# Performance work log

Measured on AMD Instinct MI355X. Metric: run time of the kernel, lower is better.

Reference implementation:

```python
import jax, jax.numpy as jnp
import numpy as np

B, D, K = 8, 128, 7          # batch, num objects, per-object feature
Q = 256                      # question embedding size
G0, G1 = 511, 512            # g-layer sizes
F1, F2, OUT = 512, 1024, 16  # f-layer sizes


def setup_inputs() -> dict:
    key = jax.random.key(0)
    ks = jax.random.split(key, 14)
    def lin(kw, kb, fan_in, fan_out):
        lim = 1.0 / np.sqrt(fan_in)
        w = jax.random.uniform(kw, (fan_in, fan_out), jnp.float32, -lim, lim)
        b = jax.random.uniform(kb, (fan_out,), jnp.float32, -lim, lim)
        return w, b
    x = jax.random.normal(ks[0], (B, D, K), jnp.float32)
    qst = jax.random.normal(ks[1], (B, Q), jnp.float32)
    g0_w, g0_b = lin(ks[2], ks[3], 2 * K, G0)
    g1_w, g1_b = lin(ks[4], ks[5], G0 + Q, G1)
    f1_w, f1_b = lin(ks[6], ks[7], G1, F1)
    f2_w, f2_b = lin(ks[8], ks[9], F1, F2)
    f3_w, f3_b = lin(ks[10], ks[11], F2, OUT)
    return {"x": x, "qst": qst,
            "g0_w": g0_w, "g0_b": g0_b, "g1_w": g1_w, "g1_b": g1_b,
            "f1_w": f1_w, "f1_b": f1_b, "f2_w": f2_w, "f2_b": f2_b,
            "f3_w": f3_w, "f3_b": f3_b}


def reference(x, qst, g0_w, g0_b, g1_w, g1_b, f1_w, f1_b, f2_w, f2_b, f3_w, f3_b):
    b, d, k = x.shape
    # all-pairs: torch x_i[b,a,c,:]=x[b,c,:], x_j[b,a,c,:]=x[b,a,:]
    x_i = jnp.broadcast_to(x[:, None, :, :], (b, d, d, k))
    x_j = jnp.broadcast_to(x[:, :, None, :], (b, d, d, k))
    pairs = jnp.concatenate([x_i, x_j], axis=-1)            # (b,d,d,2k)
    h = jax.nn.relu(pairs @ g0_w + g0_b)                    # (b,d,d,G0)
    q = jnp.broadcast_to(qst[:, None, None, :], (b, d, d, qst.shape[-1]))
    h = jnp.concatenate([h, q], axis=-1)                    # (b,d,d,G0+Q)
    h = jax.nn.relu(h @ g1_w + g1_b)                        # (b,d,d,G1)
    x_g = h.sum(axis=(1, 2))                                # sum over d^2 pairs -> (b,G1)
    f = jax.nn.relu(x_g @ f1_w + f1_b)
    f = jax.nn.relu(f @ f2_w + f2_b)                        # dropout = identity (eval)
    logits = f @ f3_w + f3_b
    return jax.nn.log_softmax(logits, axis=1)
```

## Files before the change

kernel.cpp:

```cpp
#include <hip/hip_runtime.h>
#include <hip/hip_bf16.h>

#define B_  8
#define D_  128
#define K_  7
#define Q_  256
#define G0_ 511
#define G0P 512
#define G1_ 512
#define F1_ 512
#define F2_ 1024
#define OUT_ 16

typedef __bf16 bf16x8 __attribute__((ext_vector_type(8)));
typedef float  f32x4  __attribute__((ext_vector_type(4)));

#define GL2LDS(g, l) __builtin_amdgcn_global_load_lds(                        \
    (const __attribute__((address_space(1))) void*)(g),                       \
    (__attribute__((address_space(3))) void*)(l), 16, 0, 0)

__global__ void k_prep(const float* __restrict__ x, const float* __restrict__ g0w,
                       const float* __restrict__ g0b, const float* __restrict__ qst,
                       const float* __restrict__ g1w, const float* __restrict__ g1b,
                       float* __restrict__ u, float* __restrict__ v,
                       __bf16* __restrict__ w1t, float* __restrict__ qterm,
                       float* __restrict__ xg) {
    const int blk = blockIdx.x;
    const int t   = threadIdx.x;
    if (blk < 1024) {
        __shared__ float xs[8];
        if (t < K_) xs[t] = x[blk * K_ + t];
        __syncthreads();
        #pragma unroll
        for (int h = 0; h < 2; ++h) {
            const int g = t + h * 256;
            float su = 0.f, sv = 0.f;
            if (g < G0_) {
                #pragma unroll
                for (int k = 0; k < K_; ++k) {
                    su += xs[k] * g0w[k * G0_ + g];
                    sv += xs[k] * g0w[(K_ + k) * G0_ + g];
                }
                su += g0b[g];
            }
            u[blk * G0P + g] = (g < G0_) ? su : 0.f;
            v[blk * G0P + g] = (g < G0_) ? sv : 0.f;
        }
    } else if (blk < 1280) {
        __shared__ __bf16 tile[32][33];
        const int bb = blk - 1024;
        const int bx = bb & 15, by = bb >> 4;
        const int r = t >> 5, c = t & 31;
        #pragma unroll
        for (int i = 0; i < 4; ++i) {
            const int k = by * 32 + r + i * 8;
            const int n = bx * 32 + c;
            tile[r + i * 8][c] = (__bf16)((k < G0_) ? g1w[k * G1_ + n] : 0.f);
        }
        __syncthreads();
        #pragma unroll
        for (int i = 0; i < 4; ++i) {
            const int n = bx * 32 + r + i * 8;
            const int cc = (c >> 3) & 3, j = c & 7;
            const int slot = cc ^ ((n >> 1) & 3);
            w1t[by * 16384 + n * 32 + slot * 8 + j] = tile[c][r + i * 8];
        }
    } else if (blk < 1312) {
        __shared__ float qs[256];
        __shared__ float red[2][128];
        const int qb = blk - 1280;
        const int b = qb >> 2, nb = (qb & 3) << 7;
        qs[t] = qst[b * Q_ + t];
        __syncthreads();
        const int n = nb + (t & 127);
        const int qh = (t >> 7) * 128;
        float s = 0.f;
        #pragma unroll 8
        for (int q = 0; q < 128; ++q)
            s += qs[qh + q] * g1w[(G0_ + qh + q) * G1_ + n];
        red[t >> 7][t & 127] = s;
        __syncthreads();
        if (t < 128)
            qterm[b * G1_ + nb + t] = red[0][t] + red[1][t] + g1b[nb + t];
    } else {
        const int b = blk - 1312;
        xg[b * G1_ + t] = 0.f;
        xg[b * G1_ + 256 + t] = 0.f;
    }
}

__global__ __launch_bounds__(256, 2)
void k_pair(const float* __restrict__ u, const float* __restrict__ v,
            const __bf16* __restrict__ w1t, const float* __restrict__ qterm,
            float* __restrict__ xg) {
    __shared__ float  v_a[512];
    __shared__ __bf16 At[2][4096];
    __shared__ __bf16 Bt[2][8192];
    __shared__ float  ebuf[4][128];

    const int bid  = blockIdx.x;
    const int b    = bid >> 8;
    const int a    = (bid >> 1) & 127;
    const int nbase = (bid & 1) << 8;
    const int tid  = threadIdx.x;
    const int wave = tid >> 6, lane = tid & 63;
    const int quad = lane >> 4, l15 = lane & 15;
    const int nloc = (wave >> 1) * 128;
    const int mtg  = (wave & 1) * 4;
    const int swz  = (l15 >> 1) & 3;

    if (tid < 128)
        *(float4*)(v_a + tid * 4) = *(const float4*)(v + (b * D_ + a) * G0P + tid * 4);

    const int iw0 = wave * 4;
    const __bf16* gsrc = w1t + (size_t)(nbase + iw0 * 16 + (lane >> 2)) * 32
                             + (lane & 3) * 8;

    const int sm = tid >> 1;
    const int sk = (tid & 1) << 4;
    const float* urow = u + (b * D_ + sm) * G0P + sk;
    const int woff = (sm >> 4) * 512 + (sk >> 3) * 128 + (sm & 15) * 8;

    f32x4 acc[4][8];
    #pragma unroll
    for (int mt = 0; mt < 4; ++mt)
        #pragma unroll
        for (int nt = 0; nt < 8; ++nt)
            acc[mt][nt] = (f32x4){0.f, 0.f, 0.f, 0.f};

    float4 u0, u1, u2, u3;
    auto load_u = [&](int kq) {
        const float* p = urow + kq * 32;
        u0 = *(const float4*)p;       u1 = *(const float4*)(p + 4);
        u2 = *(const float4*)(p + 8); u3 = *(const float4*)(p + 12);
    };
    auto stage_B = [&](int buf, int kq) {
        const __bf16* g = gsrc + kq * 16384;
        __bf16* l = &Bt[buf][iw0 * 512];
        #pragma unroll
        for (int j = 0; j < 4; ++j)
            GL2LDS(g + j * 512, l + j * 512);
    };
    auto write_A = [&](int buf, int kq) {
        const float* vp = v_a + kq * 32 + sk;
        const float4 v0 = *(const float4*)vp,       v1 = *(const float4*)(vp + 4);
        const float4 v2 = *(const float4*)(vp + 8), v3 = *(const float4*)(vp + 12);
        bf16x8 h0, h1;
        h0[0] = (__bf16)fmaxf(u0.x + v0.x, 0.f);
        h0[1] = (__bf16)fmaxf(u0.y + v0.y, 0.f);
        h0[2] = (__bf16)fmaxf(u0.z + v0.z, 0.f);
        h0[3] = (__bf16)fmaxf(u0.w + v0.w, 0.f);
        h0[4] = (__bf16)fmaxf(u1.x + v1.x, 0.f);
        h0[5] = (__bf16)fmaxf(u1.y + v1.y, 0.f);
        h0[6] = (__bf16)fmaxf(u1.z + v1.z, 0.f);
        h0[7] = (__bf16)fmaxf(u1.w + v1.w, 0.f);
        h1[0] = (__bf16)fmaxf(u2.x + v2.x, 0.f);
        h1[1] = (__bf16)fmaxf(u2.y + v2.y, 0.f);
        h1[2] = (__bf16)fmaxf(u2.z + v2.z, 0.f);
        h1[3] = (__bf16)fmaxf(u2.w + v2.w, 0.f);
        h1[4] = (__bf16)fmaxf(u3.x + v3.x, 0.f);
        h1[5] = (__bf16)fmaxf(u3.y + v3.y, 0.f);
        h1[6] = (__bf16)fmaxf(u3.z + v3.z, 0.f);
        h1[7] = (__bf16)fmaxf(u3.w + v3.w, 0.f);
        __bf16* w = &At[buf][woff];
        *(bf16x8*)w = h0;
        *(bf16x8*)(w + 128) = h1;
    };

    stage_B(0, 0);
    load_u(0);
    __syncthreads();
    write_A(0, 0);
    __syncthreads();

    for (int kq = 0; kq < 16; ++kq) {
        const int buf = kq & 1;
        if (kq < 15) {
            stage_B(buf ^ 1, kq + 1);
            load_u(kq + 1);
        }
        bf16x8 af[4];
        #pragma unroll
        for (int mt = 0; mt < 4; ++mt)
            af[mt] = *(const bf16x8*)&At[buf][(mtg + mt) * 512 + lane * 8];
        bf16x8 bfr[8];
        const __bf16* btb = &Bt[buf][(nloc + l15) * 32 + ((quad ^ swz) << 3)];
        #pragma unroll
        for (int nt = 0; nt < 8; ++nt)
            bfr[nt] = *(const bf16x8*)(btb + nt * 512);
        #pragma unroll
        for (int mt = 0; mt < 4; ++mt)
            #pragma unroll
            for (int nt = 0; nt < 8; ++nt)
                acc[mt][nt] = __builtin_amdgcn_mfma_f32_16x16x32_bf16(
                    af[mt], bfr[nt], acc[mt][nt], 0, 0, 0);
        if (kq < 15) write_A(buf ^ 1, kq + 1);
        __syncthreads();
    }

    #pragma unroll
    for (int nt = 0; nt < 8; ++nt) {
        const float q = qterm[b * G1_ + nbase + nloc + nt * 16 + l15];
        float s = 0.f;
        #pragma unroll
        for (int mt = 0; mt < 4; ++mt)
            #pragma unroll
            for (int r = 0; r < 4; ++r)
                s += fmaxf(acc[mt][nt][r] + q, 0.f);
        s += __shfl_xor(s, 16, 64);
        s += __shfl_xor(s, 32, 64);
        if (quad == 0) ebuf[wave][nt * 16 + l15] = s;
    }
    __syncthreads();
    {
        const int grp = tid >> 7, nl = tid & 127;
        const float sv = ebuf[grp * 2][nl] + ebuf[grp * 2 + 1][nl];
        atomicAdd(xg + b * G1_ + nbase + grp * 128 + nl, sv);
    }
}

__global__ void k_f1(const float* __restrict__ xg, const float* __restrict__ f1w,
                     const float* __restrict__ f1b, float* __restrict__ s1g) {
    const int b = blockIdx.x >> 3, ob = (blockIdx.x & 7) << 6;
    const int t = threadIdx.x;
    __shared__ float xs[512];
    __shared__ float red[4][64];
    xs[t] = xg[b * G1_ + t];
    xs[t + 256] = xg[b * G1_ + 256 + t];
    __syncthreads();
    const int o = ob + (t & 63), kq = t >> 6;
    float s = 0.f;
    #pragma unroll 8
    for (int j = 0; j < 128; ++j)
        s += xs[kq * 128 + j] * f1w[(kq * 128 + j) * F1_ + o];
    red[kq][t & 63] = s;
    __syncthreads();
    if (t < 64)
        s1g[b * F1_ + ob + t] =
            fmaxf(red[0][t] + red[1][t] + red[2][t] + red[3][t] + f1b[ob + t], 0.f);
}

__global__ void k_f2(const float* __restrict__ s1g, const float* __restrict__ f2w,
                     const float* __restrict__ f2b, float* __restrict__ s2g) {
    const int b = blockIdx.x >> 4, ob = (blockIdx.x & 15) << 6;
    const int t = threadIdx.x;
    __shared__ float xs[512];
    __shared__ float red[4][64];
    xs[t] = s1g[b * F1_ + t];
    xs[t + 256] = s1g[b * F1_ + 256 + t];
    __syncthreads();
    const int o = ob + (t & 63), kq = t >> 6;
    float s = 0.f;
    #pragma unroll 8
    for (int j = 0; j < 128; ++j)
        s += xs[kq * 128 + j] * f2w[(kq * 128 + j) * F2_ + o];
    red[kq][t & 63] = s;
    __syncthreads();
    if (t < 64)
        s2g[b * F2_ + ob + t] =
            fmaxf(red[0][t] + red[1][t] + red[2][t] + red[3][t] + f2b[ob + t], 0.f);
}

__global__ void k_f3(const float* __restrict__ s2g, const float* __restrict__ f3w,
                     const float* __restrict__ f3b, float* __restrict__ out) {
    const int b = blockIdx.x, t = threadIdx.x;
    __shared__ float xs[1024];
    __shared__ float red[16][16];
    __shared__ float lg[16];
    #pragma unroll
    for (int i = 0; i < 4; ++i) xs[t + i * 256] = s2g[b * F2_ + t + i * 256];
    __syncthreads();
    const int o = t & 15, kq = t >> 4;
    float s = 0.f;
    #pragma unroll 8
    for (int j = 0; j < 64; ++j)
        s += xs[kq * 64 + j] * f3w[(kq * 64 + j) * OUT_ + o];
    red[kq][o] = s;
    __syncthreads();
    if (t < 16) {
        float a = f3b[t];
        #pragma unroll
        for (int i = 0; i < 16; ++i) a += red[i][t];
        lg[t] = a;
    }
    __syncthreads();
    if (t < 16) {
        float m = -1e30f;
        #pragma unroll
        for (int i = 0; i < 16; ++i) m = fmaxf(m, lg[i]);
        float se = 0.f;
        #pragma unroll
        for (int i = 0; i < 16; ++i) se += __expf(lg[i] - m);
        out[b * OUT_ + t] = lg[t] - m - logf(se);
    }
}

extern "C" void kernel_launch(void* const* d_in, const int* in_sizes, int n_in,
                              void* d_out, int out_size, void* d_ws, size_t ws_size,
                              hipStream_t stream) {
    const float* x   = (const float*)d_in[0];
    const float* qst = (const float*)d_in[1];
    const float* g0w = (const float*)d_in[2];
    const float* g0b = (const float*)d_in[3];
    const float* g1w = (const float*)d_in[4];
    const float* g1b = (const float*)d_in[5];
    const float* f1w = (const float*)d_in[6];
    const float* f1b = (const float*)d_in[7];
    const float* f2w = (const float*)d_in[8];
    const float* f2b = (const float*)d_in[9];
    const float* f3w = (const float*)d_in[10];
    const float* f3b = (const float*)d_in[11];

    char* ws = (char*)d_ws;
    float*  u     = (float*)ws;  ws += (size_t)B_ * D_ * G0P * 4;
    float*  v     = (float*)ws;  ws += (size_t)B_ * D_ * G0P * 4;
    __bf16* w1t   = (__bf16*)ws; ws += (size_t)G1_ * G0P * 2;
    float*  qterm = (float*)ws;  ws += (size_t)B_ * G1_ * 4;
    float*  xg    = (float*)ws;  ws += (size_t)B_ * G1_ * 4;
    float*  s1g   = (float*)ws;  ws += (size_t)B_ * F1_ * 4;
    float*  s2g   = (float*)ws;  ws += (size_t)B_ * F2_ * 4;

    k_prep<<<1320, 256, 0, stream>>>(x, g0w, g0b, qst, g1w, g1b,
                                     u, v, w1t, qterm, xg);
    k_pair<<<B_ * D_ * 2, 256, 0, stream>>>(u, v, w1t, qterm, xg);
    k_f1  <<<64, 256, 0, stream>>>(xg, f1w, f1b, s1g);
    k_f2  <<<128, 256, 0, stream>>>(s1g, f2w, f2b, s2g);
    k_f3  <<<B_, 256, 0, stream>>>(s2g, f3w, f3b, (float*)d_out);
}
```

Measured before the change: 202.6 us.

## Transpose f-layer weights in prep and use wave-per-output dot products

Adds transpose stages to the prep kernel that write the f1, f2 and f3 weights into contiguous per-output rows. The small MLP kernels then give each wave one output and reduce a vectorized dot product with shuffles, launching many more blocks. The aim is to stop the tail MLP from running on only a few blocks with serial 128-deep loops. In exchange, each call transposes about 2.6 MB of weights and adds extra workspace traffic to the prep kernel, which runs before the pair kernel.

```diff
diff --git a/kernel.cpp b/kernel.cpp
--- a/kernel.cpp
+++ b/kernel.cpp
@@ -22,9 +22,12 @@
 __global__ void k_prep(const float* __restrict__ x, const float* __restrict__ g0w,
                        const float* __restrict__ g0b, const float* __restrict__ qst,
                        const float* __restrict__ g1w, const float* __restrict__ g1b,
+                       const float* __restrict__ f1w, const float* __restrict__ f2w,
+                       const float* __restrict__ f3w,
                        float* __restrict__ u, float* __restrict__ v,
                        __bf16* __restrict__ w1t, float* __restrict__ qterm,
-                       float* __restrict__ xg) {
+                       float* __restrict__ xg, float* __restrict__ f1t,
+                       float* __restrict__ f2t, float* __restrict__ f3t) {
     const int blk = blockIdx.x;
     const int t   = threadIdx.x;
     if (blk < 1024) {
@@ -82,10 +85,44 @@
         __syncthreads();
         if (t < 128)
             qterm[b * G1_ + nb + t] = red[0][t] + red[1][t] + g1b[nb + t];
-    } else {
+    } else if (blk < 1320) {
         const int b = blk - 1312;
         xg[b * G1_ + t] = 0.f;
         xg[b * G1_ + 256 + t] = 0.f;
+    } else if (blk < 1576) {
+        __shared__ float tile[32][33];
+        const int j = blk - 1320;
+        const int bo = j & 15, bk = j >> 4;
+        const int r = t >> 5, c = t & 31;
+        #pragma unroll
+        for (int i = 0; i < 4; ++i)
+            tile[r + i * 8][c] = f1w[(bk * 32 + r + i * 8) * F1_ + bo * 32 + c];
+        __syncthreads();
+        #pragma unroll
+        for (int i = 0; i < 4; ++i)
+            f1t[(bo * 32 + r + i * 8) * G1_ + bk * 32 + c] = tile[c][r + i * 8];
+    } else if (blk < 2088) {
+        __shared__ float tile[32][33];
+        const int j = blk - 1576;
+        const int bo = j & 31, bk = j >> 5;
+        const int r = t >> 5, c = t & 31;
+        #pragma unroll
+        for (int i = 0; i < 4; ++i)
+            tile[r + i * 8][c] = f2w[(bk * 32 + r + i * 8) * F2_ + bo * 32 + c];
+        __syncthreads();
+        #pragma unroll
+        for (int i = 0; i < 4; ++i)
+            f2t[(bo * 32 + r + i * 8) * F1_ + bk * 32 + c] = tile[c][r + i * 8];
+    } else {
+        const int k = (blk - 2088) * 256 + t;
+        float4 r0 = *(const float4*)(f3w + k * OUT_);
+        float4 r1 = *(const float4*)(f3w + k * OUT_ + 4);
+        float4 r2 = *(const float4*)(f3w + k * OUT_ + 8);
+        float4 r3 = *(const float4*)(f3w + k * OUT_ + 12);
+        const float rr[16] = {r0.x,r0.y,r0.z,r0.w, r1.x,r1.y,r1.z,r1.w,
+                              r2.x,r2.y,r2.z,r2.w, r3.x,r3.y,r3.z,r3.w};
+        #pragma unroll
+        for (int o = 0; o < 16; ++o) f3t[o * F2_ + k] = rr[o];
     }
 }
 
@@ -219,69 +256,60 @@
     }
 }
 
-__global__ void k_f1(const float* __restrict__ xg, const float* __restrict__ f1w,
+__global__ void k_f1(const float* __restrict__ xg, const float* __restrict__ f1t,
                      const float* __restrict__ f1b, float* __restrict__ s1g) {
-    const int b = blockIdx.x >> 3, ob = (blockIdx.x & 7) << 6;
-    const int t = threadIdx.x;
-    __shared__ float xs[512];
-    __shared__ float red[4][64];
-    xs[t] = xg[b * G1_ + t];
-    xs[t + 256] = xg[b * G1_ + 256 + t];
-    __syncthreads();
-    const int o = ob + (t & 63), kq = t >> 6;
-    float s = 0.f;
-    #pragma unroll 8
-    for (int j = 0; j < 128; ++j)
-        s += xs[kq * 128 + j] * f1w[(kq * 128 + j) * F1_ + o];
-    red[kq][t & 63] = s;
-    __syncthreads();
-    if (t < 64)
-        s1g[b * F1_ + ob + t] =
-            fmaxf(red[0][t] + red[1][t] + red[2][t] + red[3][t] + f1b[ob + t], 0.f);
-}
-
-__global__ void k_f2(const float* __restrict__ s1g, const float* __restrict__ f2w,
+    const int wave = threadIdx.x >> 6, lane = threadIdx.x & 63;
+    const int id = blockIdx.x * 4 + wave;
+    const int b = id >> 9, oo = id & 511;
+    const float* xr = xg + b * G1_ + lane * 8;
+    const float* wr = f1t + oo * G1_ + lane * 8;
+    const float4 a0 = *(const float4*)xr, a1 = *(const float4*)(xr + 4);
+    const float4 b0 = *(const float4*)wr, b1 = *(const float4*)(wr + 4);
+    float s = a0.x*b0.x + a0.y*b0.y + a0.z*b0.z + a0.w*b0.w
+            + a1.x*b1.x + a1.y*b1.y + a1.z*b1.z + a1.w*b1.w;
+    #pragma unroll
+    for (int off = 32; off >= 1; off >>= 1) s += __shfl_xor(s, off, 64);
+    if (lane == 0) s1g[b * F1_ + oo] = fmaxf(s + f1b[oo], 0.f);
+}
+
+__global__ void k_f2(const float* __restrict__ s1g, const float* __restrict__ f2t,
                      const float* __restrict__ f2b, float* __restrict__ s2g) {
-    const int b = blockIdx.x >> 4, ob = (blockIdx.x & 15) << 6;
-    const int t = threadIdx.x;
-    __shared__ float xs[512];
-    __shared__ float red[4][64];
-    xs[t] = s1g[b * F1_ + t];
-    xs[t + 256] = s1g[b * F1_ + 256 + t];
-    __syncthreads();
-    const int o = ob + (t & 63), kq = t >> 6;
-    float s = 0.f;
-    #pragma unroll 8
-    for (int j = 0; j < 128; ++j)
-        s += xs[kq * 128 + j] * f2w[(kq * 128 + j) * F2_ + o];
-    red[kq][t & 63] = s;
-    __syncthreads();
-    if (t < 64)
-        s2g[b * F2_ + ob + t] =
-            fmaxf(red[0][t] + red[1][t] + red[2][t] + red[3][t] + f2b[ob + t], 0.f);
-}
-
-__global__ void k_f3(const float* __restrict__ s2g, const float* __restrict__ f3w,
+    const int wave = threadIdx.x >> 6, lane = threadIdx.x & 63;
+    const int id = blockIdx.x * 4 + wave;
+    const int b = id >> 10, oo = id & 1023;
+    const float* xr = s1g + b * F1_ + lane * 8;
+    const float* wr = f2t + oo * F1_ + lane * 8;
+    const float4 a0 = *(const float4*)xr, a1 = *(const float4*)(xr + 4);
+    const float4 b0 = *(const float4*)wr, b1 = *(const float4*)(wr + 4);
+    float s = a0.x*b0.x + a0.y*b0.y + a0.z*b0.z + a0.w*b0.w
+            + a1.x*b1.x + a1.y*b1.y + a1.z*b1.z + a1.w*b1.w;
+    #pragma unroll
+    for (int off = 32; off >= 1; off >>= 1) s += __shfl_xor(s, off, 64);
+    if (lane == 0) s2g[b * F2_ + oo] = fmaxf(s + f2b[oo], 0.f);
+}
+
+__global__ void k_f3(const float* __restrict__ s2g, const float* __restrict__ f3t,
                      const float* __restrict__ f3b, float* __restrict__ out) {
     const int b = blockIdx.x, t = threadIdx.x;
-    __shared__ float xs[1024];
-    __shared__ float red[16][16];
+    const int wave = t >> 6, lane = t & 63;
     __shared__ float lg[16];
-    #pragma unroll
-    for (int i = 0; i < 4; ++i) xs[t + i * 256] = s2g[b * F2_ + t + i * 256];
-    __syncthreads();
-    const int o = t & 15, kq = t >> 4;
-    float s = 0.f;
-    #pragma unroll 8
-    for (int j = 0; j < 64; ++j)
-        s += xs[kq * 64 + j] * f3w[(kq * 64 + j) * OUT_ + o];
-    red[kq][o] = s;
-    __syncthreads();
-    if (t < 16) {
-        float a = f3b[t];
-        #pragma unroll
-        for (int i = 0; i < 16; ++i) a += red[i][t];
-        lg[t] = a;
+    float4 xs[4];
+    #pragma unroll
+    for (int j = 0; j < 4; ++j)
+        xs[j] = *(const float4*)(s2g + b * F2_ + lane * 16 + j * 4);
+    #pragma unroll
+    for (int oi = 0; oi < 4; ++oi) {
+        const int o = wave * 4 + oi;
+        const float* wr = f3t + o * F2_ + lane * 16;
+        float s = 0.f;
+        #pragma unroll
+        for (int j = 0; j < 4; ++j) {
+            const float4 w = *(const float4*)(wr + j * 4);
+            s += xs[j].x*w.x + xs[j].y*w.y + xs[j].z*w.z + xs[j].w*w.w;
+        }
+        #pragma unroll
+        for (int off = 32; off >= 1; off >>= 1) s += __shfl_xor(s, off, 64);
+        if (lane == 0) lg[o] = s + f3b[o];
     }
     __syncthreads();
     if (t < 16) {
@@ -319,11 +347,14 @@
     float*  xg    = (float*)ws;  ws += (size_t)B_ * G1_ * 4;
     float*  s1g   = (float*)ws;  ws += (size_t)B_ * F1_ * 4;
     float*  s2g   = (float*)ws;  ws += (size_t)B_ * F2_ * 4;
-
-    k_prep<<<1320, 256, 0, stream>>>(x, g0w, g0b, qst, g1w, g1b,
-                                     u, v, w1t, qterm, xg);
+    float*  f1t   = (float*)ws;  ws += (size_t)F1_ * G1_ * 4;
+    float*  f2t   = (float*)ws;  ws += (size_t)F2_ * F1_ * 4;
+    float*  f3t   = (float*)ws;  ws += (size_t)OUT_ * F2_ * 4;
+
+    k_prep<<<2092, 256, 0, stream>>>(x, g0w, g0b, qst, g1w, g1b, f1w, f2w, f3w,
+                                     u, v, w1t, qterm, xg, f1t, f2t, f3t);
     k_pair<<<B_ * D_ * 2, 256, 0, stream>>>(u, v, w1t, qterm, xg);
-    k_f1  <<<64, 256, 0, stream>>>(xg, f1w, f1b, s1g);
-    k_f2  <<<128, 256, 0, stream>>>(s1g, f2w, f2b, s2g);
-    k_f3  <<<B_, 256, 0, stream>>>(s2g, f3w, f3b, (float*)d_out);
-}
+    k_f1  <<<1024, 256, 0, stream>>>(xg, f1t, f1b, s1g);
+    k_f2  <<<2048, 256, 0, stream>>>(s1g, f2t, f2b, s2g);
+    k_f3  <<<B_, 256, 0, stream>>>(s2g, f3t, f3b, (float*)d_out);
+}
```

After: 193.5 us. -4.5%, faster.

## Process two anchor objects per pair block and fuse MLP tail into one kernel

Applied to the files above, without the earlier changes.

The pair kernel now handles two anchor objects per block, forming a 256-row A tile so each staged W1 tile feeds twice as many MFMAs. Grid size halves, accumulators double to 8x8 per wave, and launch bounds drop to one block per SIMD-pair. The three small f-layer kernels are merged into one per-batch kernel that keeps intermediates in LDS and removes two launches. Risks include register pressure and lower occupancy in the pair kernel, and the fused tail runs on only 8 blocks with serial long loops.

```diff
diff --git a/kernel.cpp b/kernel.cpp
--- a/kernel.cpp
+++ b/kernel.cpp
@@ -89,50 +89,49 @@
     }
 }
 
-__global__ __launch_bounds__(256, 2)
+__global__ __launch_bounds__(256, 1)
 void k_pair(const float* __restrict__ u, const float* __restrict__ v,
             const __bf16* __restrict__ w1t, const float* __restrict__ qterm,
             float* __restrict__ xg) {
-    __shared__ float  v_a[512];
-    __shared__ __bf16 At[2][4096];
+    __shared__ float  v_a[1024];
+    __shared__ __bf16 At[2][8192];
     __shared__ __bf16 Bt[2][8192];
     __shared__ float  ebuf[4][128];
 
     const int bid  = blockIdx.x;
-    const int b    = bid >> 8;
-    const int a    = (bid >> 1) & 127;
+    const int b    = bid >> 7;
+    const int p    = (bid >> 1) & 63;
     const int nbase = (bid & 1) << 8;
     const int tid  = threadIdx.x;
     const int wave = tid >> 6, lane = tid & 63;
     const int quad = lane >> 4, l15 = lane & 15;
-    const int nloc = (wave >> 1) * 128;
-    const int mtg  = (wave & 1) * 4;
+    const int wm = wave & 1, wn = wave >> 1;
+    const int nloc = wn * 128;
     const int swz  = (l15 >> 1) & 3;
 
-    if (tid < 128)
-        *(float4*)(v_a + tid * 4) = *(const float4*)(v + (b * D_ + a) * G0P + tid * 4);
+    *(float4*)(v_a + tid * 4) =
+        *(const float4*)(v + (b * D_ + 2 * p + (tid >> 7)) * G0P + (tid & 127) * 4);
 
     const int iw0 = wave * 4;
     const __bf16* gsrc = w1t + (size_t)(nbase + iw0 * 16 + (lane >> 2)) * 32
                              + (lane & 3) * 8;
 
-    const int sm = tid >> 1;
-    const int sk = (tid & 1) << 4;
-    const float* urow = u + (b * D_ + sm) * G0P + sk;
-    const int woff = (sm >> 4) * 512 + (sk >> 3) * 128 + (sm & 15) * 8;
-
-    f32x4 acc[4][8];
+    const int am = tid >> 7;
+    const float* urow = u + (b * D_ + (tid & 127)) * G0P;
+    const int woff = (tid >> 4) * 512 + (tid & 15) * 8;
+
+    f32x4 acc[8][8];
     #pragma unroll
-    for (int mt = 0; mt < 4; ++mt)
+    for (int mt = 0; mt < 8; ++mt)
         #pragma unroll
         for (int nt = 0; nt < 8; ++nt)
             acc[mt][nt] = (f32x4){0.f, 0.f, 0.f, 0.f};
 
-    float4 u0, u1, u2, u3;
+    float4 up[8];
     auto load_u = [&](int kq) {
-        const float* p = urow + kq * 32;
-        u0 = *(const float4*)p;       u1 = *(const float4*)(p + 4);
-        u2 = *(const float4*)(p + 8); u3 = *(const float4*)(p + 12);
+        const float* pp = urow + kq * 32;
+        #pragma unroll
+        for (int j = 0; j < 8; ++j) up[j] = *(const float4*)(pp + j * 4);
     };
     auto stage_B = [&](int buf, int kq) {
         const __bf16* g = gsrc + kq * 16384;
@@ -142,29 +141,23 @@
             GL2LDS(g + j * 512, l + j * 512);
     };
     auto write_A = [&](int buf, int kq) {
-        const float* vp = v_a + kq * 32 + sk;
-        const float4 v0 = *(const float4*)vp,       v1 = *(const float4*)(vp + 4);
-        const float4 v2 = *(const float4*)(vp + 8), v3 = *(const float4*)(vp + 12);
-        bf16x8 h0, h1;
-        h0[0] = (__bf16)fmaxf(u0.x + v0.x, 0.f);
-        h0[1] = (__bf16)fmaxf(u0.y + v0.y, 0.f);
-        h0[2] = (__bf16)fmaxf(u0.z + v0.z, 0.f);
-        h0[3] = (__bf16)fmaxf(u0.w + v0.w, 0.f);
-        h0[4] = (__bf16)fmaxf(u1.x + v1.x, 0.f);
-        h0[5] = (__bf16)fmaxf(u1.y + v1.y, 0.f);
-        h0[6] = (__bf16)fmaxf(u1.z + v1.z, 0.f);
-        h0[7] = (__bf16)fmaxf(u1.w + v1.w, 0.f);
-        h1[0] = (__bf16)fmaxf(u2.x + v2.x, 0.f);
-        h1[1] = (__bf16)fmaxf(u2.y + v2.y, 0.f);
-        h1[2] = (__bf16)fmaxf(u2.z + v2.z, 0.f);
-        h1[3] = (__bf16)fmaxf(u2.w + v2.w, 0.f);
-        h1[4] = (__bf16)fmaxf(u3.x + v3.x, 0.f);
-        h1[5] = (__bf16)fmaxf(u3.y + v3.y, 0.f);
-        h1[6] = (__bf16)fmaxf(u3.z + v3.z, 0.f);
-        h1[7] = (__bf16)fmaxf(u3.w + v3.w, 0.f);
-        __bf16* w = &At[buf][woff];
-        *(bf16x8*)w = h0;
-        *(bf16x8*)(w + 128) = h1;
+        const float* vp = v_a + am * 512 + kq * 32;
+        #pragma unroll
+        for (int q = 0; q < 4; ++q) {
+            const float4 va = *(const float4*)(vp + q * 8);
+            const float4 vb = *(const float4*)(vp + q * 8 + 4);
+            const float4 ua = up[q * 2], ub = up[q * 2 + 1];
+            bf16x8 h;
+            h[0] = (__bf16)fmaxf(ua.x + va.x, 0.f);
+            h[1] = (__bf16)fmaxf(ua.y + va.y, 0.f);
+            h[2] = (__bf16)fmaxf(ua.z + va.z, 0.f);
+            h[3] = (__bf16)fmaxf(ua.w + va.w, 0.f);
+            h[4] = (__bf16)fmaxf(ub.x + vb.x, 0.f);
+            h[5] = (__bf16)fmaxf(ub.y + vb.y, 0.f);
+            h[6] = (__bf16)fmaxf(ub.z + vb.z, 0.f);
+            h[7] = (__bf16)fmaxf(ub.w + vb.w, 0.f);
+            *(bf16x8*)&At[buf][woff + q * 128] = h;
+        }
     };
 
     stage_B(0, 0);
@@ -179,17 +172,16 @@
             stage_B(buf ^ 1, kq + 1);
             load_u(kq + 1);
         }
-        bf16x8 af[4];
-        #pragma unroll
-        for (int mt = 0; mt < 4; ++mt)
-            af[mt] = *(const bf16x8*)&At[buf][(mtg + mt) * 512 + lane * 8];
-        bf16x8 bfr[8];
+        bf16x8 af[8], bfr[8];
+        #pragma unroll
+        for (int mt = 0; mt < 8; ++mt)
+            af[mt] = *(const bf16x8*)&At[buf][(wm * 8 + mt) * 512 + lane * 8];
         const __bf16* btb = &Bt[buf][(nloc + l15) * 32 + ((quad ^ swz) << 3)];
         #pragma unroll
         for (int nt = 0; nt < 8; ++nt)
             bfr[nt] = *(const bf16x8*)(btb + nt * 512);
         #pragma unroll
-        for (int mt = 0; mt < 4; ++mt)
+        for (int mt = 0; mt < 8; ++mt)
             #pragma unroll
             for (int nt = 0; nt < 8; ++nt)
                 acc[mt][nt] = __builtin_amdgcn_mfma_f32_16x16x32_bf16(
@@ -203,7 +195,7 @@
         const float q = qterm[b * G1_ + nbase + nloc + nt * 16 + l15];
         float s = 0.f;
         #pragma unroll
-        for (int mt = 0; mt < 4; ++mt)
+        for (int mt = 0; mt < 8; ++mt)
             #pragma unroll
             for (int r = 0; r < 4; ++r)
                 s += fmaxf(acc[mt][nt][r] + q, 0.f);
@@ -214,68 +206,60 @@
     __syncthreads();
     {
         const int grp = tid >> 7, nl = tid & 127;
-        const float sv = ebuf[grp * 2][nl] + ebuf[grp * 2 + 1][nl];
-        atomicAdd(xg + b * G1_ + nbase + grp * 128 + nl, sv);
+        atomicAdd(xg + b * G1_ + nbase + grp * 128 + nl,
+                  ebuf[grp * 2][nl] + ebuf[grp * 2 + 1][nl]);
     }
 }
 
-__global__ void k_f1(const float* __restrict__ xg, const float* __restrict__ f1w,
-                     const float* __restrict__ f1b, float* __restrict__ s1g) {
-    const int b = blockIdx.x >> 3, ob = (blockIdx.x & 7) << 6;
-    const int t = threadIdx.x;
-    __shared__ float xs[512];
-    __shared__ float red[4][64];
+__global__ __launch_bounds__(256)
+void k_tail(const float* __restrict__ xg,
+            const float* __restrict__ f1w, const float* __restrict__ f1b,
+            const float* __restrict__ f2w, const float* __restrict__ f2b,
+            const float* __restrict__ f3w, const float* __restrict__ f3b,
+            float* __restrict__ out) {
+    const int b = blockIdx.x, t = threadIdx.x;
+    __shared__ float xs[G1_];
+    __shared__ float s1[F1_];
+    __shared__ float s2[F2_];
+    __shared__ float red[16][17];
+    __shared__ float lg[16];
     xs[t] = xg[b * G1_ + t];
     xs[t + 256] = xg[b * G1_ + 256 + t];
     __syncthreads();
-    const int o = ob + (t & 63), kq = t >> 6;
-    float s = 0.f;
-    #pragma unroll 8
-    for (int j = 0; j < 128; ++j)
-        s += xs[kq * 128 + j] * f1w[(kq * 128 + j) * F1_ + o];
-    red[kq][t & 63] = s;
-    __syncthreads();
-    if (t < 64)
-        s1g[b * F1_ + ob + t] =
-            fmaxf(red[0][t] + red[1][t] + red[2][t] + red[3][t] + f1b[ob + t], 0.f);
-}
-
-__global__ void k_f2(const float* __restrict__ s1g, const float* __restrict__ f2w,
-                     const float* __restrict__ f2b, float* __restrict__ s2g) {
-    const int b = blockIdx.x >> 4, ob = (blockIdx.x & 15) << 6;
-    const int t = threadIdx.x;
-    __shared__ float xs[512];
-    __shared__ float red[4][64];
-    xs[t] = s1g[b * F1_ + t];
-    xs[t + 256] = s1g[b * F1_ + 256 + t];
-    __syncthreads();
-    const int o = ob + (t & 63), kq = t >> 6;
-    float s = 0.f;
-    #pragma unroll 8
-    for (int j = 0; j < 128; ++j)
-        s += xs[kq * 128 + j] * f2w[(kq * 128 + j) * F2_ + o];
-    red[kq][t & 63] = s;
-    __syncthreads();
-    if (t < 64)
-        s2g[b * F2_ + ob + t] =
-            fmaxf(red[0][t] + red[1][t] + red[2][t] + red[3][t] + f2b[ob + t], 0.f);
-}
-
-__global__ void k_f3(const float* __restrict__ s2g, const float* __restrict__ f3w,
-                     const float* __restrict__ f3b, float* __restrict__ out) {
-    const int b = blockIdx.x, t = threadIdx.x;
-    __shared__ float xs[1024];
-    __shared__ float red[16][16];
-    __shared__ float lg[16];
-    #pragma unroll
-    for (int i = 0; i < 4; ++i) xs[t + i * 256] = s2g[b * F2_ + t + i * 256];
-    __syncthreads();
-    const int o = t & 15, kq = t >> 4;
-    float s = 0.f;
-    #pragma unroll 8
-    for (int j = 0; j < 64; ++j)
-        s += xs[kq * 64 + j] * f3w[(kq * 64 + j) * OUT_ + o];
-    red[kq][o] = s;
+    {
+        float a0 = f1b[t], a1 = f1b[t + 256];
+        #pragma unroll 8
+        for (int k = 0; k < G1_; ++k) {
+            const float xv = xs[k];
+            a0 += xv * f1w[k * F1_ + t];
+            a1 += xv * f1w[k * F1_ + t + 256];
+        }
+        s1[t] = fmaxf(a0, 0.f);
+        s1[t + 256] = fmaxf(a1, 0.f);
+    }
+    __syncthreads();
+    {
+        float4 a = *(const float4*)(f2b + t * 4);
+        #pragma unroll 8
+        for (int k = 0; k < F1_; ++k) {
+            const float sv = s1[k];
+            const float4 w = *(const float4*)(f2w + k * F2_ + t * 4);
+            a.x += sv * w.x; a.y += sv * w.y; a.z += sv * w.z; a.w += sv * w.w;
+        }
+        float4 r;
+        r.x = fmaxf(a.x, 0.f); r.y = fmaxf(a.y, 0.f);
+        r.z = fmaxf(a.z, 0.f); r.w = fmaxf(a.w, 0.f);
+        *(float4*)(s2 + t * 4) = r;
+    }
+    __syncthreads();
+    {
+        const int o = t & 15, ks = (t >> 4) * 64;
+        float a = 0.f;
+        #pragma unroll 8
+        for (int j = 0; j < 64; ++j)
+            a += s2[ks + j] * f3w[(ks + j) * OUT_ + o];
+        red[t >> 4][o] = a;
+    }
     __syncthreads();
     if (t < 16) {
         float a = f3b[t];
@@ -317,13 +301,10 @@
     __bf16* w1t   = (__bf16*)ws; ws += (size_t)G1_ * G0P * 2;
     float*  qterm = (float*)ws;  ws += (size_t)B_ * G1_ * 4;
     float*  xg    = (float*)ws;  ws += (size_t)B_ * G1_ * 4;
-    float*  s1g   = (float*)ws;  ws += (size_t)B_ * F1_ * 4;
-    float*  s2g   = (float*)ws;  ws += (size_t)B_ * F2_ * 4;
 
     k_prep<<<1320, 256, 0, stream>>>(x, g0w, g0b, qst, g1w, g1b,
                                      u, v, w1t, qterm, xg);
-    k_pair<<<B_ * D_ * 2, 256, 0, stream>>>(u, v, w1t, qterm, xg);
-    k_f1  <<<64, 256, 0, stream>>>(xg, f1w, f1b, s1g);
-    k_f2  <<<128, 256, 0, stream>>>(s1g, f2w, f2b, s2g);
-    k_f3  <<<B_, 256, 0, stream>>>(s2g, f3w, f3b, (float*)d_out);
+    k_pair<<<1024, 256, 0, stream>>>(u, v, w1t, qterm, xg);
+    k_tail<<<B_, 256, 0, stream>>>(xg, f1w, f1b, f2w, f2b, f3w, f3b,
+                                   (float*)d_out);
 }
```

New measurement: 294.6 us. +45.4%, slower.
